# Performance work log

Measured on AMD Instinct MI355X. Metric: run time of the kernel, lower is better.

The kernel has to match this reference:

```python
import jax, jax.numpy as jnp
import numpy as np

NUM_EXPERTS = 64
TOPK = 8
EPS = 1.1920929e-07  # torch.finfo(float32).eps


def setup_inputs() -> dict:
    key = jax.random.key(0)
    k1, k2 = jax.random.split(key)
    hidden_states = jax.random.normal(k1, (1, 4096, 4096), dtype=jnp.float32)
    wg_weight = jax.random.normal(k2, (NUM_EXPERTS, 4096), dtype=jnp.float32) * 0.02
    return {"hidden_states": hidden_states, "wg_weight": wg_weight}


def _routing(logits, capacity):
    # logits: [T, E]; capacity: static python int
    gates = jax.nn.softmax(logits, axis=1)                       # [T, E]
    _, idx = jax.lax.top_k(gates, TOPK)                          # [T, k]
    emask = jax.nn.one_hot(idx, NUM_EXPERTS, dtype=jnp.float32)  # [T, k, E]
    # sum of selected gate probs per token, clamped at fp32 eps
    gates_s = jnp.clip(jnp.einsum('tke,te->t', emask, gates), EPS)[:, None]
    router_probs = gates / gates_s                               # [T, E]
    # priority: cumulative position of each token within each expert,
    # scanned over (topk-major, token-minor) flattened order
    idx_flat = idx.T.reshape(-1)                                 # [k*T]
    mflat = jax.nn.one_hot(idx_flat, NUM_EXPERTS, dtype=jnp.int32)
    tp = jnp.cumsum(mflat, axis=0) * mflat - 1                   # [k*T, E]
    tp = tp.reshape(TOPK, -1, NUM_EXPERTS).transpose(1, 0, 2).max(axis=1)  # [T, E]
    valid = (tp >= 0) & (tp < capacity)                          # [T, E]
    tp = jnp.where(valid, tp, 0)
    dispatch_mask = jax.nn.one_hot(tp, capacity, dtype=jnp.bool_) & valid[:, :, None]  # [T, E, C]
    combine_weights = router_probs[:, :, None] * dispatch_mask   # [T, E, C]
    return combine_weights, dispatch_mask


def reference(hidden_states, wg_weight):
    b, s, h = hidden_states.shape
    x = hidden_states.reshape(-1, h).astype(jnp.float32)         # [T, H]
    logits = x @ wg_weight.T                                     # [T, E]
    # expert_capacity = max tokens assigned to any expert (data-dependent,
    # computed eagerly as in the torch .item() call)
    _, idx = jax.lax.top_k(jax.nn.softmax(logits, axis=1), TOPK)
    counts = jnp.bincount(idx.reshape(-1), length=NUM_EXPERTS)
    capacity = int(counts.max())
    return _routing(logits, capacity)
```

## Files before the change

kernel.cpp:

```cpp
#include <hip/hip_runtime.h>
#include <hip/hip_bf16.h>


#define TOK 4096
#define HID 4096
#define NE  64
#define NK  8
#define GEMMB 256
#define FILLB 2048

__global__ __launch_bounds__(256) void fused_gemm_fill(
    const float* __restrict__ x, const float* __restrict__ wg,
    double* __restrict__ logits, float* __restrict__ out, size_t n4,
    int* __restrict__ flag) {
  __shared__ float xs[16][68];
  __shared__ float wsh[64][68];
  const int tid = threadIdx.x;

  if ((int)blockIdx.x >= GEMMB) {
    const int fb = (int)blockIdx.x - GEMMB;
    const float4 z4 = make_float4(0.f, 0.f, 0.f, 0.f);
    float4* o4 = (float4*)out;
    for (size_t i = (size_t)fb * 256 + tid; i < n4; i += (size_t)FILLB * 256)
      o4[i] = z4;
    return;
  }

  if (blockIdx.x == 0 && tid == 0) *flag = 0;
  const int t0  = blockIdx.x * 16;
  const int tok = tid & 15;
  const int eg  = tid >> 4;
  const int lrow = tid >> 4;
  const int lq   = tid & 15;
  double acc[4] = {0.0, 0.0, 0.0, 0.0};

  for (int k0 = 0; k0 < HID; k0 += 64) {
    {
      float4 v = *(const float4*)&x[(size_t)(t0 + lrow) * HID + k0 + lq * 4];
      *(float4*)&xs[lrow][lq * 4] = v;
    }
#pragma unroll
    for (int it = 0; it < 4; ++it) {
      int r = it * 16 + lrow;
      float4 v = *(const float4*)&wg[(size_t)r * HID + k0 + lq * 4];
      *(float4*)&wsh[r][lq * 4] = v;
    }
    __syncthreads();
#pragma unroll
    for (int kk = 0; kk < 64; kk += 4) {
      float4 xv = *(const float4*)&xs[tok][kk];
#pragma unroll
      for (int j = 0; j < 4; ++j) {
        float4 wv = *(const float4*)&wsh[eg * 4 + j][kk];
        acc[j] = fma((double)xv.x, (double)wv.x, acc[j]);
        acc[j] = fma((double)xv.y, (double)wv.y, acc[j]);
        acc[j] = fma((double)xv.z, (double)wv.z, acc[j]);
        acc[j] = fma((double)xv.w, (double)wv.w, acc[j]);
      }
    }
    __syncthreads();
  }
#pragma unroll
  for (int j = 0; j < 4; ++j)
    logits[(size_t)(t0 + tok) * NE + eg * 4 + j] = acc[j];
}

__global__ __launch_bounds__(256) void verify_kernel(
    const float* __restrict__ x, const float* __restrict__ wg,
    const double* __restrict__ logits, int* __restrict__ flag) {
  const int gid  = blockIdx.x * blockDim.x + threadIdx.x;
  const int wid  = gid >> 6;
  const int lane = gid & 63;
  const int t = (wid * 521) & (TOK - 1);
  const int e = wid & 63;
  double acc = 0.0;
  for (int k = lane; k < HID; k += 64)
    acc = fma((double)x[(size_t)t * HID + k], (double)wg[(size_t)e * HID + k], acc);
#pragma unroll
  for (int off = 32; off; off >>= 1) acc += __shfl_xor(acc, off);
  if (lane == 0) {
    double got = logits[(size_t)t * NE + e];
    if (!(fabs(got - acc) <= 1e-6)) atomicOr(flag, 1);
  }
}

__global__ __launch_bounds__(256) void repair_gemm(
    const float* __restrict__ x, const float* __restrict__ wg,
    double* __restrict__ logits, const int* __restrict__ flag) {
  if (*(volatile const int*)flag == 0) return;
  const int gid = blockIdx.x * 256 + threadIdx.x;
  const int t = gid >> 6;
  const int e = gid & 63;
  double a0 = 0, a1 = 0, a2 = 0, a3 = 0, a4 = 0, a5 = 0, a6 = 0, a7 = 0;
  const float* xr = x  + (size_t)t * HID;
  const float* wr = wg + (size_t)e * HID;
  for (int k = 0; k < HID; k += 8) {
    float4 xv0 = *(const float4*)&xr[k];
    float4 xv1 = *(const float4*)&xr[k + 4];
    float4 wv0 = *(const float4*)&wr[k];
    float4 wv1 = *(const float4*)&wr[k + 4];
    a0 = fma((double)xv0.x, (double)wv0.x, a0);
    a1 = fma((double)xv0.y, (double)wv0.y, a1);
    a2 = fma((double)xv0.z, (double)wv0.z, a2);
    a3 = fma((double)xv0.w, (double)wv0.w, a3);
    a4 = fma((double)xv1.x, (double)wv1.x, a4);
    a5 = fma((double)xv1.y, (double)wv1.y, a5);
    a6 = fma((double)xv1.z, (double)wv1.z, a6);
    a7 = fma((double)xv1.w, (double)wv1.w, a7);
  }
  logits[(size_t)t * NE + e] = ((((((a0 + a1) + a2) + a3) + a4) + a5) + a6) + a7;
}

__global__ __launch_bounds__(256) void topk_kernel(
    const double* __restrict__ logits,
    int* __restrict__ idx_kt, float* __restrict__ w_kt) {
  const int gid  = blockIdx.x * blockDim.x + threadIdx.x;
  const int t    = gid >> 6;
  const int lane = gid & 63;

  double v = logits[(size_t)t * NE + lane];

  double m = v;
#pragma unroll
  for (int off = 32; off; off >>= 1) {
    double o = __shfl_xor(m, off);
    m = o > m ? o : m;
  }
  double g = exp(v - m);
  double s = g;
#pragma unroll
  for (int off = 32; off; off >>= 1) s += __shfl_xor(s, off);
  double gate = g / s;

  float key = (float)gate;
  double ssel = 0.0;
  int my_k = -1;
#pragma unroll
  for (int k = 0; k < NK; ++k) {
    float bv = key;
    int   bi = lane;
#pragma unroll
    for (int off = 32; off; off >>= 1) {
      float ov = __shfl_xor(bv, off);
      int   oi = __shfl_xor(bi, off);
      if (ov > bv || (ov == bv && oi < bi)) { bv = ov; bi = oi; }
    }
    ssel += __shfl(gate, bi);
    if (lane == bi) { my_k = k; key = -1.0f; }
  }
  double gs = ssel;
  const double eps = (double)1.1920929e-07f;
  if (gs < eps) gs = eps;

  if (my_k >= 0) {
    idx_kt[my_k * TOK + t] = lane;
    w_kt [my_k * TOK + t] = (float)(gate / gs);
  }
}

__global__ __launch_bounds__(1024) void rank_kernel(
    const int* __restrict__ idx_kt, int* __restrict__ rank_kt) {
  const int e    = blockIdx.x;
  const int tid  = threadIdx.x;
  const int lane = tid & 63;
  const int w    = tid >> 6;
  __shared__ int wt[16];
  int running = 0;
  const unsigned long long below = (1ull << lane) - 1ull;

  for (int i0 = 0; i0 < NK * TOK; i0 += 1024) {
    const int i = i0 + tid;
    const bool mhit = (idx_kt[i] == e);
    unsigned long long mask = __ballot(mhit);
    if (lane == 0) wt[w] = __popcll(mask);
    __syncthreads();
    int woff = 0, tot = 0;
#pragma unroll
    for (int j = 0; j < 16; ++j) {
      int c = wt[j];
      tot += c;
      if (j < w) woff += c;
    }
    if (mhit) rank_kt[i] = running + woff + __popcll(mask & below);
    running += tot;
    __syncthreads();
  }
}

__global__ __launch_bounds__(256) void scatter_kernel(
    const int* __restrict__ idx_kt, const int* __restrict__ rank_kt,
    const float* __restrict__ w_kt, float* __restrict__ out, int C) {
  const int i = blockIdx.x * 256 + threadIdx.x;
  const int t = i & (TOK - 1);
  const int e = idx_kt[i];
  const int c = rank_kt[i];
  const float wv = w_kt[i];
  if (e >= 0 && e < NE && c >= 0 && c < C) {
    size_t off = ((size_t)t * NE + e) * (size_t)C + (size_t)c;
    out[off] = wv;
    out[(size_t)TOK * NE * C + off] = 1.0f;
  }
}

extern "C" void kernel_launch(void* const* d_in, const int* in_sizes, int n_in,
                              void* d_out, int out_size, void* d_ws, size_t ws_size,
                              hipStream_t stream) {
  const float* x  = (const float*)d_in[0];
  const float* wg = (const float*)d_in[1];
  float* out = (float*)d_out;

  const int C = out_size / (2 * TOK * NE);

  char* ws = (char*)d_ws;
  double* logits  = (double*)ws;
  int*    idx_kt  = (int*)  (ws + (size_t)2 * 1024 * 1024);
  int*    rank_kt = (int*)  (ws + (size_t)2 * 1024 * 1024 + (size_t)NK * TOK * 4);
  float*  w_kt    = (float*)(ws + (size_t)2 * 1024 * 1024 + (size_t)NK * TOK * 8);
  int*    flag    = (int*)  (ws + (size_t)2 * 1024 * 1024 + (size_t)NK * TOK * 12);

  const size_t n4 = (size_t)out_size >> 2;

  fused_gemm_fill<<<GEMMB + FILLB, 256, 0, stream>>>(x, wg, logits, out, n4, flag);
  verify_kernel  <<<128, 256, 0, stream>>>(x, wg, logits, flag);
  repair_gemm    <<<TOK * NE / 256, 256, 0, stream>>>(x, wg, logits, flag);
  topk_kernel    <<<TOK * 64 / 256, 256, 0, stream>>>(logits, idx_kt, w_kt);
  rank_kernel    <<<NE, 1024, 0, stream>>>(idx_kt, rank_kt);
  scatter_kernel <<<NK * TOK / 256, 256, 0, stream>>>(idx_kt, rank_kt, w_kt, out, C);
}
```

Measured before the change: 1.316 ms.

## Split-K the gating GEMM, memset output separately, fuse rank and scatter

The FP64-accumulated gating GEMM moves from 256 blocks to a 2D grid that splits the K dimension into up to 8 chunks. Each chunk writes a partial-logit slab, and the top-k and verify kernels sum the slabs. The zero fill of the output, previously done by extra blocks inside the GEMM launch, becomes a hipMemsetAsync. The rank kernel now writes the scatter outputs directly, which removes the separate scatter kernel and the rank buffer. In exchange it needs more workspace, adds partial reads in top-k, and serializes the memset before the GEMM instead of overlapping them.

```diff
diff --git a/kernel.cpp b/kernel.cpp
--- a/kernel.cpp
+++ b/kernel.cpp
@@ -6,52 +6,41 @@
 #define HID 4096
 #define NE  64
 #define NK  8
-#define GEMMB 256
-#define FILLB 2048
-
-__global__ __launch_bounds__(256) void fused_gemm_fill(
+
+__global__ __launch_bounds__(256) void gemm_splitk(
     const float* __restrict__ x, const float* __restrict__ wg,
-    double* __restrict__ logits, float* __restrict__ out, size_t n4,
-    int* __restrict__ flag) {
+    double* __restrict__ partial, int kchunk, int* __restrict__ flag) {
   __shared__ float xs[16][68];
   __shared__ float wsh[64][68];
   const int tid = threadIdx.x;
-
-  if ((int)blockIdx.x >= GEMMB) {
-    const int fb = (int)blockIdx.x - GEMMB;
-    const float4 z4 = make_float4(0.f, 0.f, 0.f, 0.f);
-    float4* o4 = (float4*)out;
-    for (size_t i = (size_t)fb * 256 + tid; i < n4; i += (size_t)FILLB * 256)
-      o4[i] = z4;
-    return;
-  }
-
-  if (blockIdx.x == 0 && tid == 0) *flag = 0;
+  if (blockIdx.x == 0 && blockIdx.y == 0 && tid == 0) *flag = 0;
   const int t0  = blockIdx.x * 16;
+  const int k0  = blockIdx.y * kchunk;
   const int tok = tid & 15;
   const int eg  = tid >> 4;
   const int lrow = tid >> 4;
   const int lq   = tid & 15;
   double acc[4] = {0.0, 0.0, 0.0, 0.0};
 
-  for (int k0 = 0; k0 < HID; k0 += 64) {
+  for (int s = 0; s < kchunk; s += 64) {
+    const int kk = k0 + s;
     {
-      float4 v = *(const float4*)&x[(size_t)(t0 + lrow) * HID + k0 + lq * 4];
+      float4 v = *(const float4*)&x[(size_t)(t0 + lrow) * HID + kk + lq * 4];
       *(float4*)&xs[lrow][lq * 4] = v;
     }
 #pragma unroll
     for (int it = 0; it < 4; ++it) {
       int r = it * 16 + lrow;
-      float4 v = *(const float4*)&wg[(size_t)r * HID + k0 + lq * 4];
+      float4 v = *(const float4*)&wg[(size_t)r * HID + kk + lq * 4];
       *(float4*)&wsh[r][lq * 4] = v;
     }
     __syncthreads();
 #pragma unroll
-    for (int kk = 0; kk < 64; kk += 4) {
-      float4 xv = *(const float4*)&xs[tok][kk];
+    for (int kc = 0; kc < 64; kc += 4) {
+      float4 xv = *(const float4*)&xs[tok][kc];
 #pragma unroll
       for (int j = 0; j < 4; ++j) {
-        float4 wv = *(const float4*)&wsh[eg * 4 + j][kk];
+        float4 wv = *(const float4*)&wsh[eg * 4 + j][kc];
         acc[j] = fma((double)xv.x, (double)wv.x, acc[j]);
         acc[j] = fma((double)xv.y, (double)wv.y, acc[j]);
         acc[j] = fma((double)xv.z, (double)wv.z, acc[j]);
@@ -60,14 +49,15 @@
     }
     __syncthreads();
   }
+  double* base = partial + (size_t)blockIdx.y * TOK * NE;
 #pragma unroll
   for (int j = 0; j < 4; ++j)
-    logits[(size_t)(t0 + tok) * NE + eg * 4 + j] = acc[j];
+    base[(size_t)(t0 + tok) * NE + eg * 4 + j] = acc[j];
 }
 
 __global__ __launch_bounds__(256) void verify_kernel(
     const float* __restrict__ x, const float* __restrict__ wg,
-    const double* __restrict__ logits, int* __restrict__ flag) {
+    const double* __restrict__ partial, int nsplit, int* __restrict__ flag) {
   const int gid  = blockIdx.x * blockDim.x + threadIdx.x;
   const int wid  = gid >> 6;
   const int lane = gid & 63;
@@ -79,14 +69,16 @@
 #pragma unroll
   for (int off = 32; off; off >>= 1) acc += __shfl_xor(acc, off);
   if (lane == 0) {
-    double got = logits[(size_t)t * NE + e];
+    double got = 0.0;
+    for (int p = 0; p < nsplit; ++p)
+      got += partial[(size_t)p * TOK * NE + (size_t)t * NE + e];
     if (!(fabs(got - acc) <= 1e-6)) atomicOr(flag, 1);
   }
 }
 
 __global__ __launch_bounds__(256) void repair_gemm(
     const float* __restrict__ x, const float* __restrict__ wg,
-    double* __restrict__ logits, const int* __restrict__ flag) {
+    double* __restrict__ partial, int nsplit, const int* __restrict__ flag) {
   if (*(volatile const int*)flag == 0) return;
   const int gid = blockIdx.x * 256 + threadIdx.x;
   const int t = gid >> 6;
@@ -108,17 +100,22 @@
     a6 = fma((double)xv1.z, (double)wv1.z, a6);
     a7 = fma((double)xv1.w, (double)wv1.w, a7);
   }
-  logits[(size_t)t * NE + e] = ((((((a0 + a1) + a2) + a3) + a4) + a5) + a6) + a7;
+  partial[(size_t)t * NE + e] =
+      ((((((a0 + a1) + a2) + a3) + a4) + a5) + a6) + a7;
+  for (int p = 1; p < nsplit; ++p)
+    partial[(size_t)p * TOK * NE + (size_t)t * NE + e] = 0.0;
 }
 
 __global__ __launch_bounds__(256) void topk_kernel(
-    const double* __restrict__ logits,
+    const double* __restrict__ partial, int nsplit,
     int* __restrict__ idx_kt, float* __restrict__ w_kt) {
   const int gid  = blockIdx.x * blockDim.x + threadIdx.x;
   const int t    = gid >> 6;
   const int lane = gid & 63;
 
-  double v = logits[(size_t)t * NE + lane];
+  double v = 0.0;
+  for (int p = 0; p < nsplit; ++p)
+    v += partial[(size_t)p * TOK * NE + (size_t)t * NE + lane];
 
   double m = v;
 #pragma unroll
@@ -158,8 +155,9 @@
   }
 }
 
-__global__ __launch_bounds__(1024) void rank_kernel(
-    const int* __restrict__ idx_kt, int* __restrict__ rank_kt) {
+__global__ __launch_bounds__(1024) void rank_scatter(
+    const int* __restrict__ idx_kt, const float* __restrict__ w_kt,
+    float* __restrict__ out, int C) {
   const int e    = blockIdx.x;
   const int tid  = threadIdx.x;
   const int lane = tid & 63;
@@ -181,24 +179,17 @@
       tot += c;
       if (j < w) woff += c;
     }
-    if (mhit) rank_kt[i] = running + woff + __popcll(mask & below);
+    if (mhit) {
+      const int c = running + woff + __popcll(mask & below);
+      if (c < C) {
+        const int t = i & (TOK - 1);
+        size_t off = ((size_t)t * NE + e) * (size_t)C + (size_t)c;
+        out[off] = w_kt[i];
+        out[(size_t)TOK * NE * C + off] = 1.0f;
+      }
+    }
     running += tot;
     __syncthreads();
-  }
-}
-
-__global__ __launch_bounds__(256) void scatter_kernel(
-    const int* __restrict__ idx_kt, const int* __restrict__ rank_kt,
-    const float* __restrict__ w_kt, float* __restrict__ out, int C) {
-  const int i = blockIdx.x * 256 + threadIdx.x;
-  const int t = i & (TOK - 1);
-  const int e = idx_kt[i];
-  const int c = rank_kt[i];
-  const float wv = w_kt[i];
-  if (e >= 0 && e < NE && c >= 0 && c < C) {
-    size_t off = ((size_t)t * NE + e) * (size_t)C + (size_t)c;
-    out[off] = wv;
-    out[(size_t)TOK * NE * C + off] = 1.0f;
   }
 }
 
@@ -211,19 +202,24 @@
 
   const int C = out_size / (2 * TOK * NE);
 
+  const size_t slab = (size_t)TOK * NE * sizeof(double);
+  const size_t tail = 2 * (size_t)NK * TOK * sizeof(int);
+  int nsplit = 8;
+  while (nsplit > 1 && (size_t)nsplit * slab + tail + 64 > ws_size) nsplit >>= 1;
+  const int kchunk = HID / nsplit;
+
   char* ws = (char*)d_ws;
-  double* logits  = (double*)ws;
-  int*    idx_kt  = (int*)  (ws + (size_t)2 * 1024 * 1024);
-  int*    rank_kt = (int*)  (ws + (size_t)2 * 1024 * 1024 + (size_t)NK * TOK * 4);
-  float*  w_kt    = (float*)(ws + (size_t)2 * 1024 * 1024 + (size_t)NK * TOK * 8);
-  int*    flag    = (int*)  (ws + (size_t)2 * 1024 * 1024 + (size_t)NK * TOK * 12);
-
-  const size_t n4 = (size_t)out_size >> 2;
-
-  fused_gemm_fill<<<GEMMB + FILLB, 256, 0, stream>>>(x, wg, logits, out, n4, flag);
-  verify_kernel  <<<128, 256, 0, stream>>>(x, wg, logits, flag);
-  repair_gemm    <<<TOK * NE / 256, 256, 0, stream>>>(x, wg, logits, flag);
-  topk_kernel    <<<TOK * 64 / 256, 256, 0, stream>>>(logits, idx_kt, w_kt);
-  rank_kernel    <<<NE, 1024, 0, stream>>>(idx_kt, rank_kt);
-  scatter_kernel <<<NK * TOK / 256, 256, 0, stream>>>(idx_kt, rank_kt, w_kt, out, C);
-}
+  double* partial = (double*)ws;
+  int*    idx_kt  = (int*)  (ws + (size_t)nsplit * slab);
+  float*  w_kt    = (float*)(ws + (size_t)nsplit * slab + (size_t)NK * TOK * 4);
+  int*    flag    = (int*)  (ws + (size_t)nsplit * slab + tail);
+
+  hipMemsetAsync(d_out, 0, (size_t)out_size * sizeof(float), stream);
+
+  dim3 ggrid(TOK / 16, nsplit);
+  gemm_splitk <<<ggrid, 256, 0, stream>>>(x, wg, partial, kchunk, flag);
+  verify_kernel<<<128, 256, 0, stream>>>(x, wg, partial, nsplit, flag);
+  repair_gemm <<<TOK * NE / 256, 256, 0, stream>>>(x, wg, partial, nsplit, flag);
+  topk_kernel <<<TOK * 64 / 256, 256, 0, stream>>>(partial, nsplit, idx_kt, w_kt);
+  rank_scatter<<<NE, 1024, 0, stream>>>(idx_kt, w_kt, out, C);
+}
```

New measurement: 1.296 ms. About the same (-1.5%).
